# Kernel tuning notes

Measured on AMD Instinct MI355X. Metric: run time of the kernel, lower is better.

## Reference

```python
import jax, jax.numpy as jnp
import numpy as np

B, I, J, WIDTH, NH = 8, 1024, 1024, 512, 8
HD = WIDTH // NH
SCALE = WIDTH ** (-0.5)  # NOTE: original scales by width**-0.5, not head_dim**-0.5


def setup_inputs() -> dict:
    key = jax.random.key(0)
    ks = jax.random.split(key, 7)
    return {
        "q": jax.random.normal(ks[0], (B, I, WIDTH), dtype=jnp.float32),
        "k": jax.random.normal(ks[1], (B, J, WIDTH), dtype=jnp.float32),
        "v": jax.random.normal(ks[2], (B, J, WIDTH), dtype=jnp.float32),
        "Wq": jax.random.normal(ks[3], (WIDTH, WIDTH), dtype=jnp.float32) * (WIDTH ** -0.5),
        "Wk": jax.random.normal(ks[4], (WIDTH, WIDTH), dtype=jnp.float32) * (WIDTH ** -0.5),
        "Wv": jax.random.normal(ks[5], (WIDTH, WIDTH), dtype=jnp.float32) * (WIDTH ** -0.5),
        "Wo": jax.random.normal(ks[6], (WIDTH, WIDTH), dtype=jnp.float32) * (WIDTH ** -0.5),
    }


def reference(q, k, v, Wq, Wk, Wv, Wo):
    b, i, _ = q.shape
    j = k.shape[1]
    # Linear(bias=False): y = x @ W.T
    qh = (q @ Wq.T).reshape(b, NH, i, HD)  # faithful to torch .view(b, n, i, d) (no transpose)
    kh = (k @ Wk.T).reshape(b, NH, j, HD)
    vh = (v @ Wv.T).reshape(b, NH, j, HD)
    attn_score = jnp.einsum('bnid,bnjd->bnij', qh, kh) * SCALE
    attn_weight = jax.nn.softmax(attn_score, axis=3)
    # drop_prob = 0.0 -> dropout is identity
    x = jnp.einsum('bnij,bnjd->bnid', attn_weight, vh)
    x = x.transpose(0, 2, 1, 3).reshape(b, i, NH * HD)  # b n i d -> b i (n d)
    x = x @ Wo.T
    return (x, attn_weight)
```

## Files before the change

kernel.cpp:

```cpp
#include <hip/hip_runtime.h>
#include <hip/hip_bf16.h>


typedef __hip_bfloat16 bf16;
typedef __attribute__((ext_vector_type(8))) short bf16x8;
typedef __attribute__((ext_vector_type(4))) float f32x4;

#define BATCH 8
#define SEQ   1024
#define WIDTH 512
#define NHEAD 8
#define HD    64
#define SCALE_F 0.044194173824159216f

static __device__ __forceinline__ unsigned short f2bf(float x) {
  union { float f; unsigned u; } a; a.f = x;
  unsigned r = a.u + 0x7fffu + ((a.u >> 16) & 1u);
  return (unsigned short)(r >> 16);
}
static __device__ __forceinline__ float bf2f(unsigned short u) {
  union { unsigned u; float f; } a; a.u = ((unsigned)u) << 16; return a.f;
}

static __device__ __forceinline__ void gload_lds16(const void* g, void* l) {
  __builtin_amdgcn_global_load_lds((const __attribute__((address_space(1))) void*)g,
                                   (__attribute__((address_space(3))) void*)l,
                                   16, 0, 0);
}

static __device__ __forceinline__ bf16x8 frag_ld(const short* tile, int row, int c16) {
  int p = c16 ^ (row & 7);
  return *(const bf16x8*)(tile + row*64 + p*8);
}

__global__ void cast_all_kernel(const float* __restrict__ q, const float* __restrict__ k,
                                const float* __restrict__ v, const float* __restrict__ wq,
                                const float* __restrict__ wk, const float* __restrict__ wv,
                                const float* __restrict__ wo, bf16* __restrict__ wsb) {
  const long NQ = 1048576;
  const long NW = 65536;
  long g = (long)blockIdx.x * blockDim.x + threadIdx.x;
  const float* src; bf16* dst; long o;
  if (g < 3*NQ) {
    int t = (int)(g / NQ); o = g - (long)t*NQ;
    src = (t==0) ? q : ((t==1) ? k : v);
    dst = wsb + (size_t)t * 4194304;
  } else {
    long g2 = g - 3*NQ;
    if (g2 >= 4*NW) return;
    int t = (int)(g2 / NW); o = g2 - (long)t*NW;
    src = (t==0) ? wq : ((t==1) ? wk : ((t==2) ? wv : wo));
    dst = wsb + (size_t)3*4194304 + (size_t)t * 262144;
  }
  float4 f = ((const float4*)src)[o];
  ushort4 r4;
  r4.x = f2bf(f.x); r4.y = f2bf(f.y); r4.z = f2bf(f.z); r4.w = f2bf(f.w);
  ((ushort4*)dst)[o] = r4;
}

__global__ __launch_bounds__(256) void gemm_qkv(const bf16* __restrict__ A0, const bf16* __restrict__ A1,
                                                const bf16* __restrict__ A2, const bf16* __restrict__ W0,
                                                const bf16* __restrict__ W1, const bf16* __restrict__ W2,
                                                bf16* __restrict__ C0, bf16* __restrict__ C1,
                                                bf16* __restrict__ C2) {
  __shared__ short As[2][128*64];
  __shared__ short Bs[2][128*64];

  const int bid = blockIdx.x;
  const int xcd = bid & 7;
  const int idx = bid >> 3;
  const int g   = xcd*24 + (idx >> 2);
  const int y   = idx & 3;
  const int z   = g >> 6;
  const int m   = g & 63;

  const bf16* A  = (z==0) ? A0 : ((z==1) ? A1 : A2);
  const bf16* Bw = (z==0) ? W0 : ((z==1) ? W1 : W2);
  bf16* Cout     = (z==0) ? C0 : ((z==1) ? C1 : C2);

  const int lane = threadIdx.x & 63;
  const int wid  = threadIdx.x >> 6;
  const int m0 = m * 128;
  const int n0 = y * 128;
  const int wm = (wid >> 1) * 64;
  const int wn = (wid & 1) * 64;
  const int lrow = lane >> 3;
  const int swz  = ((lane & 7) ^ lrow) * 8;

  const f32x4 zero4 = {0.f,0.f,0.f,0.f};
  f32x4 acc[4][4];
  for (int i=0;i<4;++i) for (int j=0;j<4;++j) acc[i][j] = zero4;

  auto stage = [&](int buf, int t) {
    const int k0 = t * 64;
    for (int i = 0; i < 4; ++i) {
      int c = wid*4 + i;
      int row = c*8 + lrow;
      gload_lds16(A  + (size_t)(m0 + row)*WIDTH + k0 + swz, &As[buf][c*512]);
      gload_lds16(Bw + (size_t)(n0 + row)*WIDTH + k0 + swz, &Bs[buf][c*512]);
    }
  };

  stage(0, 0);
  asm volatile("s_waitcnt vmcnt(0)" ::: "memory");
  __syncthreads();
  int cur = 0;

  for (int t = 0; t < 8; ++t) {
    if (t < 7) stage(cur ^ 1, t + 1);
    for (int kc = 0; kc < 2; ++kc) {
      bf16x8 af[4], bfr[4];
      for (int mf=0; mf<4; ++mf) af[mf]  = frag_ld(&As[cur][0], wm + mf*16 + (lane&15), (lane>>4) + kc*4);
      for (int nf=0; nf<4; ++nf) bfr[nf] = frag_ld(&Bs[cur][0], wn + nf*16 + (lane&15), (lane>>4) + kc*4);
      for (int mf=0; mf<4; ++mf)
        for (int nf=0; nf<4; ++nf)
          acc[mf][nf] = __builtin_amdgcn_mfma_f32_16x16x32_bf16(af[mf], bfr[nf], acc[mf][nf], 0,0,0);
    }
    if (t < 7) {
      asm volatile("s_waitcnt vmcnt(0)" ::: "memory");
      __syncthreads();
      cur ^= 1;
    }
  }
  for (int mf=0; mf<4; ++mf)
    for (int nf=0; nf<4; ++nf) {
      int col = n0 + wn + nf*16 + (lane & 15);
      for (int r=0; r<4; ++r) {
        int row = m0 + wm + mf*16 + (lane>>4)*4 + r;
        ((unsigned short*)Cout)[(size_t)row*WIDTH + col] = f2bf(acc[mf][nf][r]);
      }
    }
}

__global__ __launch_bounds__(256) void gemm_out(const bf16* __restrict__ A,
                                                const bf16* __restrict__ Bw,
                                                float* __restrict__ Cout) {
  __shared__ short As[2][128*64];
  __shared__ short Bs[2][64*64];

  const int bid = blockIdx.x;
  const int xcd = bid & 7;
  const int idx = bid >> 3;
  const int m   = xcd*8 + (idx >> 3);
  const int y   = idx & 7;

  const int lane = threadIdx.x & 63;
  const int wid  = threadIdx.x >> 6;
  const int m0 = m * 128;
  const int n0 = y * 64;
  const int wm = (wid >> 1) * 64;
  const int wn = (wid & 1) * 32;
  const int lrow = lane >> 3;
  const int swz  = ((lane & 7) ^ lrow) * 8;

  const f32x4 zero4 = {0.f,0.f,0.f,0.f};
  f32x4 acc[4][2];
  for (int i=0;i<4;++i) for (int j=0;j<2;++j) acc[i][j] = zero4;

  auto stage = [&](int buf, int t) {
    const int k0 = t * 64;
    for (int i = 0; i < 4; ++i) {
      int c = wid*4 + i;
      int row = c*8 + lrow;
      gload_lds16(A + (size_t)(m0 + row)*WIDTH + k0 + swz, &As[buf][c*512]);
    }
    for (int i = 0; i < 2; ++i) {
      int c = wid*2 + i;
      int row = c*8 + lrow;
      gload_lds16(Bw + (size_t)(n0 + row)*WIDTH + k0 + swz, &Bs[buf][c*512]);
    }
  };

  stage(0, 0);
  asm volatile("s_waitcnt vmcnt(0)" ::: "memory");
  __syncthreads();
  int cur = 0;

  for (int t = 0; t < 8; ++t) {
    if (t < 7) stage(cur ^ 1, t + 1);
    for (int kc = 0; kc < 2; ++kc) {
      bf16x8 af[4], bfr[2];
      for (int mf=0; mf<4; ++mf) af[mf]  = frag_ld(&As[cur][0], wm + mf*16 + (lane&15), (lane>>4) + kc*4);
      for (int nf=0; nf<2; ++nf) bfr[nf] = frag_ld(&Bs[cur][0], wn + nf*16 + (lane&15), (lane>>4) + kc*4);
      for (int mf=0; mf<4; ++mf)
        for (int nf=0; nf<2; ++nf)
          acc[mf][nf] = __builtin_amdgcn_mfma_f32_16x16x32_bf16(af[mf], bfr[nf], acc[mf][nf], 0,0,0);
    }
    if (t < 7) {
      asm volatile("s_waitcnt vmcnt(0)" ::: "memory");
      __syncthreads();
      cur ^= 1;
    }
  }
  for (int mf=0; mf<4; ++mf)
    for (int nf=0; nf<2; ++nf) {
      int col = n0 + wn + nf*16 + (lane & 15);
      for (int r=0; r<4; ++r) {
        int row = m0 + wm + mf*16 + (lane>>4)*4 + r;
        __builtin_nontemporal_store(acc[mf][nf][r], Cout + (size_t)row*WIDTH + col);
      }
    }
}

__global__ __launch_bounds__(256) void transpose_v(const bf16* __restrict__ Vh,
                                                   bf16* __restrict__ Vt) {
  __shared__ short t[64][72];
  int h  = blockIdx.x >> 4;
  int j0 = (blockIdx.x & 15) * 64;
  const bf16* src = Vh + (size_t)h * (SEQ*HD);
  bf16* dst = Vt + (size_t)h * (SEQ*HD);
  int tid = threadIdx.x;
  int r  = tid >> 2;
  int c0 = (tid & 3) * 16;
  bf16x8 v0 = *(const bf16x8*)(src + (size_t)(j0 + r)*HD + c0);
  bf16x8 v1 = *(const bf16x8*)(src + (size_t)(j0 + r)*HD + c0 + 8);
  for (int i = 0; i < 8; ++i) { t[r][c0+i] = v0[i]; t[r][c0+8+i] = v1[i]; }
  __syncthreads();
  bf16x8 w0, w1;
  for (int i = 0; i < 8; ++i) { w0[i] = t[c0+i][r]; w1[i] = t[c0+8+i][r]; }
  *(bf16x8*)(dst + (size_t)r*SEQ + j0 + c0)     = w0;
  *(bf16x8*)(dst + (size_t)r*SEQ + j0 + c0 + 8) = w1;
}

__global__ __launch_bounds__(512) void attn_kernel(const bf16* __restrict__ Qh,
                                                   const bf16* __restrict__ Kh,
                                                   const bf16* __restrict__ Vt,
                                                   float* __restrict__ attn_out,
                                                   bf16* __restrict__ ctx) {
  __shared__ short Ks[2][128*64];
  __shared__ short Vs[2][128*64];
  __shared__ short Ws[8][16*64];

  const int lane = threadIdx.x & 63;
  const int wid  = threadIdx.x >> 6;
  const int bid  = blockIdx.x;
  const int xcd  = bid & 7;
  const int idx  = bid >> 3;
  const int h    = xcd*8 + (idx >> 3);
  const int i0   = (idx & 7) * 128;
  const int b  = h >> 3;
  const int nh = h & 7;

  const bf16* Qhead  = Qh + (size_t)h * (SEQ*HD);
  const bf16* Khead  = Kh + (size_t)h * (SEQ*HD);
  const bf16* Vthead = Vt + (size_t)h * (SEQ*HD);

  const int lrow = lane >> 3;
  const int swz  = ((lane & 7) ^ lrow) * 8;

  const int qrow = i0 + wid*16 + (lane & 15);
  bf16x8 qf[2];
  qf[0] = *(const bf16x8*)(Qhead + (size_t)qrow*HD + (lane>>4)*8);
  qf[1] = *(const bf16x8*)(Qhead + (size_t)qrow*HD + 32 + (lane>>4)*8);

  const f32x4 zero4 = {0.f,0.f,0.f,0.f};

  auto stageK = [&](int buf, int jt) {
    const int j0 = jt * 128;
    for (int i = 0; i < 2; ++i) {
      int c = wid*2 + i;
      gload_lds16(Khead + (size_t)(j0 + c*8 + lrow)*HD + swz, &Ks[buf][c*512]);
    }
  };
  auto stageV = [&](int buf, int jt) {
    const int j0 = jt * 128;
    for (int i = 0; i < 2; ++i) {
      int c = wid*2 + i;
      int sub = c >> 3, dr = (c & 7)*8 + lrow;
      gload_lds16(Vthead + (size_t)dr*SEQ + j0 + sub*64 + swz, &Vs[buf][c*512]);
    }
  };

  float lsum[4] = {0.f,0.f,0.f,0.f};
  stageK(0, 0);
  asm volatile("s_waitcnt vmcnt(0)" ::: "memory");
  __syncthreads();
  int cur = 0;
  for (int jt = 0; jt < 8; ++jt) {
    if (jt < 7) stageK(cur ^ 1, jt + 1);
    #pragma unroll
    for (int half = 0; half < 2; ++half) {
      const short* Kt = &Ks[cur][half*4096];
      f32x4 sac[4] = {zero4, zero4, zero4, zero4};
      __builtin_amdgcn_s_setprio(1);
      for (int kc = 0; kc < 2; ++kc)
        for (int jf = 0; jf < 4; ++jf) {
          bf16x8 kf = frag_ld(Kt, jf*16 + (lane & 15), (lane>>4) + kc*4);
          sac[jf] = __builtin_amdgcn_mfma_f32_16x16x32_bf16(qf[kc], kf, sac[jf], 0, 0, 0);
        }
      __builtin_amdgcn_s_setprio(0);
      for (int jf = 0; jf < 4; ++jf)
        for (int r = 0; r < 4; ++r)
          lsum[r] += __expf(sac[jf][r] * SCALE_F);
    }
    if (jt < 7) {
      asm volatile("s_waitcnt vmcnt(0)" ::: "memory");
      __syncthreads();
      cur ^= 1;
    }
  }
  for (int m = 1; m < 16; m <<= 1)
    for (int r = 0; r < 4; ++r)
      lsum[r] += __shfl_xor(lsum[r], m, 64);
  float linv[4];
  for (int r = 0; r < 4; ++r) linv[r] = 1.0f / lsum[r];
  __syncthreads();

  f32x4 cacc[4] = {zero4, zero4, zero4, zero4};
  short* Wsw = &Ws[wid][0];
  float* awbase = attn_out + (size_t)((size_t)h*SEQ + i0 + wid*16)*SEQ;
  stageK(0, 0); stageV(0, 0);
  asm volatile("s_waitcnt vmcnt(0)" ::: "memory");
  __syncthreads();
  cur = 0;
  for (int jt = 0; jt < 8; ++jt) {
    if (jt < 7) { stageK(cur ^ 1, jt + 1); stageV(cur ^ 1, jt + 1); }
    const int j0 = jt * 128;
    #pragma unroll
    for (int half = 0; half < 2; ++half) {
      const short* Kt  = &Ks[cur][half*4096];
      const short* Vtt = &Vs[cur][half*4096];
      f32x4 sac[4] = {zero4, zero4, zero4, zero4};
      __builtin_amdgcn_s_setprio(1);
      for (int kc = 0; kc < 2; ++kc)
        for (int jf = 0; jf < 4; ++jf) {
          bf16x8 kf = frag_ld(Kt, jf*16 + (lane & 15), (lane>>4) + kc*4);
          sac[jf] = __builtin_amdgcn_mfma_f32_16x16x32_bf16(qf[kc], kf, sac[jf], 0, 0, 0);
        }
      __builtin_amdgcn_s_setprio(0);
      for (int jf = 0; jf < 4; ++jf)
        for (int r = 0; r < 4; ++r) {
          float w = __expf(sac[jf][r] * SCALE_F) * linv[r];
          int row = (lane>>4)*4 + r;
          int col = jf*16 + (lane & 15);
          Wsw[row*64 + (((col>>3) ^ (row & 7))<<3) + (col & 7)] = (short)f2bf(w);
        }
      asm volatile("s_waitcnt lgkmcnt(0)" ::: "memory");
      __builtin_amdgcn_s_setprio(1);
      for (int kc = 0; kc < 2; ++kc) {
        bf16x8 wa = frag_ld(Wsw, lane & 15, (lane>>4) + kc*4);
        for (int df = 0; df < 4; ++df) {
          bf16x8 vb = frag_ld(Vtt, df*16 + (lane & 15), (lane>>4) + kc*4);
          cacc[df] = __builtin_amdgcn_mfma_f32_16x16x32_bf16(wa, vb, cacc[df], 0, 0, 0);
        }
      }
      __builtin_amdgcn_s_setprio(0);
      #pragma unroll
      for (int s = 0; s < 4; ++s) {
        int row = (lane>>4) + s*4;
        int lu  = (lane & 15) >> 1;
        uint2 pv = *(const uint2*)(Wsw + row*64 + ((lu ^ (row & 7)) << 3) + (lane & 1)*4);
        f32x4 o;
        o[0] = bf2f((unsigned short)(pv.x & 0xffff));
        o[1] = bf2f((unsigned short)(pv.x >> 16));
        o[2] = bf2f((unsigned short)(pv.y & 0xffff));
        o[3] = bf2f((unsigned short)(pv.y >> 16));
        __builtin_nontemporal_store(o,
            (f32x4*)(awbase + (size_t)row*SEQ + j0 + half*64 + (lane & 15)*4));
      }
    }
    if (jt < 7) {
      asm volatile("s_waitcnt vmcnt(8) lgkmcnt(0)" ::: "memory");
      __builtin_amdgcn_s_barrier();
      cur ^= 1;
    }
  }
  for (int df = 0; df < 4; ++df)
    for (int r = 0; r < 4; ++r) {
      int irow = i0 + wid*16 + (lane>>4)*4 + r;
      ((unsigned short*)ctx)[(size_t)(b*SEQ + irow)*WIDTH + nh*HD + df*16 + (lane & 15)]
          = f2bf(cacc[df][r]);
    }
}

extern "C" void kernel_launch(void* const* d_in, const int* in_sizes, int n_in,
                              void* d_out, int out_size, void* d_ws, size_t ws_size,
                              hipStream_t stream) {
  const float* q  = (const float*)d_in[0];
  const float* k  = (const float*)d_in[1];
  const float* v  = (const float*)d_in[2];
  const float* wq = (const float*)d_in[3];
  const float* wk = (const float*)d_in[4];
  const float* wv = (const float*)d_in[5];
  const float* wo = (const float*)d_in[6];

  bf16* wsb = (bf16*)d_ws;
  bf16* qb  = wsb;
  bf16* kb  = qb + 4194304;
  bf16* vb  = kb + 4194304;
  bf16* wqb = vb + 4194304;
  bf16* wkb = wqb + 262144;
  bf16* wvb = wkb + 262144;
  bf16* wob = wvb + 262144;
  bf16* Qh  = wob + 262144;
  bf16* Kh  = Qh + 4194304;
  bf16* Vh  = Kh + 4194304;
  bf16* Vt  = Vh + 4194304;
  bf16* ctx = Vt + 4194304;

  float* x_out    = (float*)d_out;
  float* attn_out = (float*)d_out + 4194304;

  cast_all_kernel<<<13312, 256, 0, stream>>>(q, k, v, wq, wk, wv, wo, wsb);
  gemm_qkv<<<768, 256, 0, stream>>>(qb, kb, vb, wqb, wkb, wvb, Qh, Kh, Vh);
  transpose_v<<<1024, 256, 0, stream>>>(Vh, Vt);
  attn_kernel<<<512, 512, 0, stream>>>(Qh, Kh, Vt, attn_out, ctx);
  gemm_out<<<512, 256, 0, stream>>>(ctx, wob, x_out);
}
```

Before: 129.3 us.

## Load K fragments directly from global memory instead of staging through LDS

Removes the double-buffered LDS staging of K tiles in both softmax passes. Each lane now loads its K MFMA fragments straight from global memory into registers, relying on L2/L1 reuse across the 8 waves. This cuts LDS footprint (possibly raising occupancy) and drops the per-tile barriers and waitcnts in the first pass. In exchange there are more global loads with less coalescing and exposed load latency before the MFMAs.

```diff
diff --git a/kernel.cpp b/kernel.cpp
--- a/kernel.cpp
+++ b/kernel.cpp
@@ -227,7 +227,6 @@
                                                    const bf16* __restrict__ Vt,
                                                    float* __restrict__ attn_out,
                                                    bf16* __restrict__ ctx) {
-  __shared__ short Ks[2][128*64];
   __shared__ short Vs[2][128*64];
   __shared__ short Ws[8][16*64];
 
@@ -254,14 +253,9 @@
   qf[1] = *(const bf16x8*)(Qhead + (size_t)qrow*HD + 32 + (lane>>4)*8);
 
   const f32x4 zero4 = {0.f,0.f,0.f,0.f};
-
-  auto stageK = [&](int buf, int jt) {
-    const int j0 = jt * 128;
-    for (int i = 0; i < 2; ++i) {
-      int c = wid*2 + i;
-      gload_lds16(Khead + (size_t)(j0 + c*8 + lrow)*HD + swz, &Ks[buf][c*512]);
-    }
-  };
+  const int kjl = lane & 15;
+  const int kd0 = (lane >> 4) * 8;
+
   auto stageV = [&](int buf, int jt) {
     const int j0 = jt * 128;
     for (int i = 0; i < 2; ++i) {
@@ -272,63 +266,65 @@
   };
 
   float lsum[4] = {0.f,0.f,0.f,0.f};
-  stageK(0, 0);
-  asm volatile("s_waitcnt vmcnt(0)" ::: "memory");
-  __syncthreads();
-  int cur = 0;
-  for (int jt = 0; jt < 8; ++jt) {
-    if (jt < 7) stageK(cur ^ 1, jt + 1);
+  #pragma unroll 2
+  for (int jt = 0; jt < 16; ++jt) {
+    const int j0 = jt * 64;
+    bf16x8 kfr[8];
     #pragma unroll
-    for (int half = 0; half < 2; ++half) {
-      const short* Kt = &Ks[cur][half*4096];
-      f32x4 sac[4] = {zero4, zero4, zero4, zero4};
-      __builtin_amdgcn_s_setprio(1);
-      for (int kc = 0; kc < 2; ++kc)
-        for (int jf = 0; jf < 4; ++jf) {
-          bf16x8 kf = frag_ld(Kt, jf*16 + (lane & 15), (lane>>4) + kc*4);
-          sac[jf] = __builtin_amdgcn_mfma_f32_16x16x32_bf16(qf[kc], kf, sac[jf], 0, 0, 0);
-        }
-      __builtin_amdgcn_s_setprio(0);
+    for (int kc = 0; kc < 2; ++kc)
+      #pragma unroll
       for (int jf = 0; jf < 4; ++jf)
-        for (int r = 0; r < 4; ++r)
-          lsum[r] += __expf(sac[jf][r] * SCALE_F);
-    }
-    if (jt < 7) {
-      asm volatile("s_waitcnt vmcnt(0)" ::: "memory");
-      __syncthreads();
-      cur ^= 1;
-    }
+        kfr[kc*4+jf] = *(const bf16x8*)(Khead + (size_t)(j0 + jf*16 + kjl)*HD + kd0 + kc*32);
+    f32x4 sac[4] = {zero4, zero4, zero4, zero4};
+    __builtin_amdgcn_s_setprio(1);
+    #pragma unroll
+    for (int kc = 0; kc < 2; ++kc)
+      #pragma unroll
+      for (int jf = 0; jf < 4; ++jf)
+        sac[jf] = __builtin_amdgcn_mfma_f32_16x16x32_bf16(qf[kc], kfr[kc*4+jf], sac[jf], 0, 0, 0);
+    __builtin_amdgcn_s_setprio(0);
+    #pragma unroll
+    for (int jf = 0; jf < 4; ++jf)
+      #pragma unroll
+      for (int r = 0; r < 4; ++r)
+        lsum[r] += __expf(sac[jf][r] * SCALE_F);
   }
   for (int m = 1; m < 16; m <<= 1)
     for (int r = 0; r < 4; ++r)
       lsum[r] += __shfl_xor(lsum[r], m, 64);
   float linv[4];
   for (int r = 0; r < 4; ++r) linv[r] = 1.0f / lsum[r];
-  __syncthreads();
 
   f32x4 cacc[4] = {zero4, zero4, zero4, zero4};
   short* Wsw = &Ws[wid][0];
   float* awbase = attn_out + (size_t)((size_t)h*SEQ + i0 + wid*16)*SEQ;
-  stageK(0, 0); stageV(0, 0);
+  stageV(0, 0);
   asm volatile("s_waitcnt vmcnt(0)" ::: "memory");
   __syncthreads();
-  cur = 0;
+  int cur = 0;
   for (int jt = 0; jt < 8; ++jt) {
-    if (jt < 7) { stageK(cur ^ 1, jt + 1); stageV(cur ^ 1, jt + 1); }
+    if (jt < 7) stageV(cur ^ 1, jt + 1);
     const int j0 = jt * 128;
     #pragma unroll
     for (int half = 0; half < 2; ++half) {
-      const short* Kt  = &Ks[cur][half*4096];
       const short* Vtt = &Vs[cur][half*4096];
+      bf16x8 kfr[8];
+      #pragma unroll
+      for (int kc = 0; kc < 2; ++kc)
+        #pragma unroll
+        for (int jf = 0; jf < 4; ++jf)
+          kfr[kc*4+jf] = *(const bf16x8*)(Khead + (size_t)(j0 + half*64 + jf*16 + kjl)*HD + kd0 + kc*32);
       f32x4 sac[4] = {zero4, zero4, zero4, zero4};
       __builtin_amdgcn_s_setprio(1);
+      #pragma unroll
       for (int kc = 0; kc < 2; ++kc)
-        for (int jf = 0; jf < 4; ++jf) {
-          bf16x8 kf = frag_ld(Kt, jf*16 + (lane & 15), (lane>>4) + kc*4);
-          sac[jf] = __builtin_amdgcn_mfma_f32_16x16x32_bf16(qf[kc], kf, sac[jf], 0, 0, 0);
-        }
+        #pragma unroll
+        for (int jf = 0; jf < 4; ++jf)
+          sac[jf] = __builtin_amdgcn_mfma_f32_16x16x32_bf16(qf[kc], kfr[kc*4+jf], sac[jf], 0, 0, 0);
       __builtin_amdgcn_s_setprio(0);
+      #pragma unroll
       for (int jf = 0; jf < 4; ++jf)
+        #pragma unroll
         for (int r = 0; r < 4; ++r) {
           float w = __expf(sac[jf][r] * SCALE_F) * linv[r];
           int row = (lane>>4)*4 + r;
@@ -337,8 +333,10 @@
         }
       asm volatile("s_waitcnt lgkmcnt(0)" ::: "memory");
       __builtin_amdgcn_s_setprio(1);
+      #pragma unroll
       for (int kc = 0; kc < 2; ++kc) {
         bf16x8 wa = frag_ld(Wsw, lane & 15, (lane>>4) + kc*4);
+        #pragma unroll
         for (int df = 0; df < 4; ++df) {
           bf16x8 vb = frag_ld(Vtt, df*16 + (lane & 15), (lane>>4) + kc*4);
           cacc[df] = __builtin_amdgcn_mfma_f32_16x16x32_bf16(wa, vb, cacc[df], 0, 0, 0);
```

Result: slower. 185.1 us (+43.2%).

## Fuse fp32-to-bf16 activation cast into QKV GEMM, cast only weights separately

Applied to the files above, without the earlier changes.

The separate cast of q, k and v to bf16 is removed. The QKV GEMM now stages fp32 activation tiles into LDS and converts them to bf16 in registers with v_cvt_pk_bf16_f32 before the MFMA. This removes a full read and write of the three activation tensors and shrinks the cast kernel to the weights only. In exchange the K tile halves to 32, doubling the loop iterations and barriers, and the GEMM now reads fp32 activations from global memory.

```diff
diff --git a/kernel.cpp b/kernel.cpp
--- a/kernel.cpp
+++ b/kernel.cpp
@@ -33,38 +33,35 @@
   return *(const bf16x8*)(tile + row*64 + p*8);
 }
 
-__global__ void cast_all_kernel(const float* __restrict__ q, const float* __restrict__ k,
-                                const float* __restrict__ v, const float* __restrict__ wq,
-                                const float* __restrict__ wk, const float* __restrict__ wv,
-                                const float* __restrict__ wo, bf16* __restrict__ wsb) {
-  const long NQ = 1048576;
+static __device__ __forceinline__ unsigned cvtpk(float a, float b) {
+  unsigned d;
+  asm("v_cvt_pk_bf16_f32 %0, %1, %2" : "=v"(d) : "v"(a), "v"(b));
+  return d;
+}
+
+__global__ void wcast_kernel(const float* __restrict__ wq, const float* __restrict__ wk,
+                             const float* __restrict__ wv, const float* __restrict__ wo,
+                             bf16* __restrict__ wsb) {
   const long NW = 65536;
   long g = (long)blockIdx.x * blockDim.x + threadIdx.x;
-  const float* src; bf16* dst; long o;
-  if (g < 3*NQ) {
-    int t = (int)(g / NQ); o = g - (long)t*NQ;
-    src = (t==0) ? q : ((t==1) ? k : v);
-    dst = wsb + (size_t)t * 4194304;
-  } else {
-    long g2 = g - 3*NQ;
-    if (g2 >= 4*NW) return;
-    int t = (int)(g2 / NW); o = g2 - (long)t*NW;
-    src = (t==0) ? wq : ((t==1) ? wk : ((t==2) ? wv : wo));
-    dst = wsb + (size_t)3*4194304 + (size_t)t * 262144;
-  }
+  int t = (int)(g / NW); long o = g - (long)t*NW;
+  const float* src = (t==0) ? wq : ((t==1) ? wk : ((t==2) ? wv : wo));
+  bf16* dst = wsb + (size_t)t * 262144;
   float4 f = ((const float4*)src)[o];
   ushort4 r4;
   r4.x = f2bf(f.x); r4.y = f2bf(f.y); r4.z = f2bf(f.z); r4.w = f2bf(f.w);
   ((ushort4*)dst)[o] = r4;
 }
 
-__global__ __launch_bounds__(256) void gemm_qkv(const bf16* __restrict__ A0, const bf16* __restrict__ A1,
-                                                const bf16* __restrict__ A2, const bf16* __restrict__ W0,
-                                                const bf16* __restrict__ W1, const bf16* __restrict__ W2,
-                                                bf16* __restrict__ C0, bf16* __restrict__ C1,
-                                                bf16* __restrict__ C2) {
-  __shared__ short As[2][128*64];
-  __shared__ short Bs[2][128*64];
+__global__ __launch_bounds__(256) void gemm_qkv(const float* __restrict__ Aq,
+                                                const float* __restrict__ Ak,
+                                                const float* __restrict__ Av,
+                                                const bf16* __restrict__ Wb,
+                                                bf16* __restrict__ Qh,
+                                                bf16* __restrict__ Kh,
+                                                bf16* __restrict__ Vh) {
+  __shared__ float Af[2][128*32];
+  __shared__ short Bs[2][128*32];
 
   const int bid = blockIdx.x;
   const int xcd = bid & 7;
@@ -74,9 +71,9 @@
   const int z   = g >> 6;
   const int m   = g & 63;
 
-  const bf16* A  = (z==0) ? A0 : ((z==1) ? A1 : A2);
-  const bf16* Bw = (z==0) ? W0 : ((z==1) ? W1 : W2);
-  bf16* Cout     = (z==0) ? C0 : ((z==1) ? C1 : C2);
+  const float* A = (z==0) ? Aq : ((z==1) ? Ak : Av);
+  const bf16* Bw = Wb + (size_t)z * 262144;
+  bf16* Cout     = (z==0) ? Qh : ((z==1) ? Kh : Vh);
 
   const int lane = threadIdx.x & 63;
   const int wid  = threadIdx.x >> 6;
@@ -84,20 +81,27 @@
   const int n0 = y * 128;
   const int wm = (wid >> 1) * 64;
   const int wn = (wid & 1) * 64;
-  const int lrow = lane >> 3;
-  const int swz  = ((lane & 7) ^ lrow) * 8;
+
+  const int lrowA = lane >> 3;
+  const int luA   = lane & 7;
+  const int lrowB = lane >> 2;
+  const int luB   = lane & 3;
 
   const f32x4 zero4 = {0.f,0.f,0.f,0.f};
   f32x4 acc[4][4];
   for (int i=0;i<4;++i) for (int j=0;j<4;++j) acc[i][j] = zero4;
 
   auto stage = [&](int buf, int t) {
-    const int k0 = t * 64;
+    const int k0 = t * 32;
     for (int i = 0; i < 4; ++i) {
       int c = wid*4 + i;
-      int row = c*8 + lrow;
-      gload_lds16(A  + (size_t)(m0 + row)*WIDTH + k0 + swz, &As[buf][c*512]);
-      gload_lds16(Bw + (size_t)(n0 + row)*WIDTH + k0 + swz, &Bs[buf][c*512]);
+      int row = c*8 + lrowA;
+      gload_lds16(A + (size_t)(m0 + row)*WIDTH + k0 + ((luA ^ lrowA) * 4), &Af[buf][c*256]);
+    }
+    for (int i = 0; i < 2; ++i) {
+      int c = wid*2 + i;
+      int row = c*16 + lrowB;
+      gload_lds16(Bw + (size_t)(n0 + row)*WIDTH + k0 + ((luB ^ (lrowB & 3)) * 8), &Bs[buf][c*512]);
     }
   };
 
@@ -106,17 +110,36 @@
   __syncthreads();
   int cur = 0;
 
-  for (int t = 0; t < 8; ++t) {
-    if (t < 7) stage(cur ^ 1, t + 1);
-    for (int kc = 0; kc < 2; ++kc) {
-      bf16x8 af[4], bfr[4];
-      for (int mf=0; mf<4; ++mf) af[mf]  = frag_ld(&As[cur][0], wm + mf*16 + (lane&15), (lane>>4) + kc*4);
-      for (int nf=0; nf<4; ++nf) bfr[nf] = frag_ld(&Bs[cur][0], wn + nf*16 + (lane&15), (lane>>4) + kc*4);
-      for (int mf=0; mf<4; ++mf)
-        for (int nf=0; nf<4; ++nf)
-          acc[mf][nf] = __builtin_amdgcn_mfma_f32_16x16x32_bf16(af[mf], bfr[nf], acc[mf][nf], 0,0,0);
-    }
-    if (t < 7) {
+  const int kg = lane >> 4;
+  for (int t = 0; t < 16; ++t) {
+    if (t < 15) stage(cur ^ 1, t + 1);
+    bf16x8 af[4], bfr[4];
+    #pragma unroll
+    for (int mf = 0; mf < 4; ++mf) {
+      int row = wm + mf*16 + (lane & 15);
+      const float* rp = &Af[cur][row*32];
+      f32x4 lo = *(const f32x4*)(rp + (((2*kg)   ^ (row & 7)) * 4));
+      f32x4 hi = *(const f32x4*)(rp + (((2*kg+1) ^ (row & 7)) * 4));
+      unsigned d0 = cvtpk(lo[0], lo[1]);
+      unsigned d1 = cvtpk(lo[2], lo[3]);
+      unsigned d2 = cvtpk(hi[0], hi[1]);
+      unsigned d3 = cvtpk(hi[2], hi[3]);
+      af[mf][0] = (short)(d0 & 0xffff); af[mf][1] = (short)(d0 >> 16);
+      af[mf][2] = (short)(d1 & 0xffff); af[mf][3] = (short)(d1 >> 16);
+      af[mf][4] = (short)(d2 & 0xffff); af[mf][5] = (short)(d2 >> 16);
+      af[mf][6] = (short)(d3 & 0xffff); af[mf][7] = (short)(d3 >> 16);
+    }
+    #pragma unroll
+    for (int nf = 0; nf < 4; ++nf) {
+      int row = wn + nf*16 + (lane & 15);
+      bfr[nf] = *(const bf16x8*)(&Bs[cur][row*32 + ((kg ^ (row & 3)) * 8)]);
+    }
+    #pragma unroll
+    for (int mf = 0; mf < 4; ++mf)
+      #pragma unroll
+      for (int nf = 0; nf < 4; ++nf)
+        acc[mf][nf] = __builtin_amdgcn_mfma_f32_16x16x32_bf16(af[mf], bfr[nf], acc[mf][nf], 0,0,0);
+    if (t < 15) {
       asm volatile("s_waitcnt vmcnt(0)" ::: "memory");
       __syncthreads();
       cur ^= 1;
@@ -385,14 +408,9 @@
   const float* wo = (const float*)d_in[6];
 
   bf16* wsb = (bf16*)d_ws;
-  bf16* qb  = wsb;
-  bf16* kb  = qb + 4194304;
-  bf16* vb  = kb + 4194304;
-  bf16* wqb = vb + 4194304;
-  bf16* wkb = wqb + 262144;
-  bf16* wvb = wkb + 262144;
-  bf16* wob = wvb + 262144;
-  bf16* Qh  = wob + 262144;
+  bf16* wqb = wsb;
+  bf16* wob = wqb + 3*262144;
+  bf16* Qh  = wqb + 4*262144;
   bf16* Kh  = Qh + 4194304;
   bf16* Vh  = Kh + 4194304;
   bf16* Vt  = Vh + 4194304;
@@ -401,8 +419,8 @@
   float* x_out    = (float*)d_out;
   float* attn_out = (float*)d_out + 4194304;
 
-  cast_all_kernel<<<13312, 256, 0, stream>>>(q, k, v, wq, wk, wv, wo, wsb);
-  gemm_qkv<<<768, 256, 0, stream>>>(qb, kb, vb, wqb, wkb, wvb, Qh, Kh, Vh);
+  wcast_kernel<<<1024, 256, 0, stream>>>(wq, wk, wv, wo, wqb);
+  gemm_qkv<<<768, 256, 0, stream>>>(q, k, v, wqb, Qh, Kh, Vh);
   transpose_v<<<1024, 256, 0, stream>>>(Vh, Vt);
   attn_kernel<<<512, 512, 0, stream>>>(Qh, Kh, Vt, attn_out, ctx);
   gemm_out<<<512, 256, 0, stream>>>(ctx, wob, x_out);
```

After: 124.1 us. -4.0%, faster.
